# Kernel optimization log

Hardware: AMD Instinct MI355X
Metric: run time of the kernel (lower is better)

Reference implementation:

```python
import jax, jax.numpy as jnp
import numpy as np

WS = 3          # window size (odd)
NH = 8          # num heads
EPS = 1e-5      # LayerNorm eps (torch default)


def _ln(x, g, b):
    mu = x.mean(-1, keepdims=True)
    var = ((x - mu) ** 2).mean(-1, keepdims=True)
    return (x - mu) / jnp.sqrt(var + EPS) * g + b


def _neighbors(x, ws):
    # x: [B,D,H,W,C] -> [B,D,H,W,ws^3,C] zero-padded cubic neighborhoods
    B, D, H, W, C = x.shape
    r = ws // 2
    xp = jnp.pad(x, ((0, 0), (r, r), (r, r), (r, r), (0, 0)))
    slabs = [xp[:, i:i + D, j:j + H, k:k + W, :]
             for i in range(ws) for j in range(ws) for k in range(ws)]
    return jnp.stack(slabs, axis=4)


def _mask(D, H, W, ws):
    # True for valid (in-bounds, non-center) neighbors: [D,H,W,ws^3]
    r = ws // 2
    valid = jnp.pad(jnp.ones((D, H, W), dtype=bool), ((r, r), (r, r), (r, r)))
    slabs = [valid[i:i + D, j:j + H, k:k + W]
             for i in range(ws) for j in range(ws) for k in range(ws)]
    m = jnp.stack(slabs, axis=3)
    center = r * ws * ws + r * ws + r  # self voxel is masked out
    return m.at[..., center].set(False)


def setup_inputs() -> dict:
    key = jax.random.key(0)
    ks = jax.random.split(key, 18)
    B, D, H, W, C = 2, 16, 16, 16, 256
    F = 4 * C
    s = 0.02
    inp = {
        "x": jax.random.normal(ks[0], (B, D, H, W, C), jnp.float32),
        "Wq": jax.random.normal(ks[1], (C, C), jnp.float32) * s,
        "bq": jnp.zeros((C,), jnp.float32),
        "Wk": jax.random.normal(ks[2], (C, C), jnp.float32) * s,
        "bk": jnp.zeros((C,), jnp.float32),
        "Wv": jax.random.normal(ks[3], (C, C), jnp.float32) * s,
        "bv": jnp.zeros((C,), jnp.float32),
        "Wo": jax.random.normal(ks[4], (C, C), jnp.float32) * s,
        "bo": jnp.zeros((C,), jnp.float32),
        "g1": jnp.ones((C,), jnp.float32),
        "b1": jnp.zeros((C,), jnp.float32),
        "g2": jnp.ones((C,), jnp.float32),
        "b2": jnp.zeros((C,), jnp.float32),
        "W1": jax.random.normal(ks[5], (C, F), jnp.float32) * s,
        "bf1": jnp.zeros((F,), jnp.float32),
        "W2": jax.random.normal(ks[6], (F, C), jnp.float32) * s,
        "bf2": jnp.zeros((C,), jnp.float32),
    }
    return inp


def reference(x, Wq, bq, Wk, bk, Wv, bv, Wo, bo, g1, b1, g2, b2, W1, bf1, W2, bf2):
    B, D, H, W, C = x.shape
    ws, nh = WS, NH
    hd = C // nh
    K = ws ** 3

    nb = _neighbors(x, ws)                                   # [B,D,H,W,K,C]
    m = _mask(D, H, W, ws)                                   # [D,H,W,K]

    tn = _ln(x, g1, b1)                                      # norm1 on target only
    q = (tn @ Wq + bq).reshape(B, D, H, W, nh, hd)
    k = (nb @ Wk + bk).reshape(B, D, H, W, K, nh, hd)        # keys from RAW neighbors
    v = (nb @ Wv + bv).reshape(B, D, H, W, K, nh, hd)

    scale = hd ** -0.5
    scores = jnp.einsum('bpqrne,bpqrkne->bpqrnk', q, k) * scale  # [B,D,H,W,nh,K]
    mb = m[None, :, :, :, None, :]
    scores = jnp.where(mb, scores, -jnp.inf)
    attn = jax.nn.softmax(scores, axis=-1)
    attn = jnp.where(jnp.isnan(attn), jnp.zeros_like(attn), attn)

    ao = jnp.einsum('bpqrnk,bpqrkne->bpqrne', attn, v).reshape(B, D, H, W, C)
    ao = ao @ Wo + bo

    t = x + ao                                                # residual (dropout = eval identity)
    h = jax.nn.gelu(_ln(t, g2, b2) @ W1 + bf1, approximate=False) @ W2 + bf2
    return t + h
```

## Files before the change

### kernel.cpp

```cpp
#include <hip/hip_runtime.h>

typedef __bf16 bf16x8 __attribute__((ext_vector_type(8)));
typedef float f32x4 __attribute__((ext_vector_type(4)));

#define DEV static __device__ __forceinline__

DEV unsigned short f2b(float f){
    unsigned int u = __float_as_uint(f);
    u += 0x7fffu + ((u >> 16) & 1u);
    return (unsigned short)(u >> 16);
}
DEV float b2f(unsigned short h){ return __uint_as_float(((unsigned int)h) << 16); }
DEV float blo(unsigned int u){ return __uint_as_float(u << 16); }
DEV float bhi(unsigned int u){ return __uint_as_float(u & 0xffff0000u); }
DEV float gelu_f(float x){ return 0.5f * x * (1.0f + erff(x * 0.7071067811865476f)); }

DEV void gload16(const unsigned short* g, unsigned short* l){
    __builtin_amdgcn_global_load_lds(
        (const __attribute__((address_space(1))) void*)g,
        (__attribute__((address_space(3))) void*)l, 16, 0, 0);
}

static constexpr int NROW = 8192;
static constexpr int C    = 256;
static constexpr int F    = 1024;
static constexpr float ATT_SCALE = 0.17677669529663688f;

__global__ __launch_bounds__(256)
void prep_ln_kernel(const float* __restrict__ Wq, const float* __restrict__ Wk,
                    const float* __restrict__ Wv, const float* __restrict__ Wo,
                    const float* __restrict__ W1, const float* __restrict__ W2,
                    const float* __restrict__ bq, const float* __restrict__ bk,
                    const float* __restrict__ bv,
                    unsigned short* __restrict__ WQT, unsigned short* __restrict__ WKT,
                    unsigned short* __restrict__ WVT, unsigned short* __restrict__ WOT,
                    unsigned short* __restrict__ W1T, unsigned short* __restrict__ W2T,
                    float* __restrict__ bqkv,
                    const float* __restrict__ x, const float* __restrict__ g1,
                    const float* __restrict__ b1,
                    unsigned short* __restrict__ tn, unsigned short* __restrict__ xb)
{
    const int tid = threadIdx.x;
    if (blockIdx.x < 192) {
        __shared__ unsigned short T[64][66];
        const int t = blockIdx.x;
        const float* src; unsigned short* dst;
        int ldw, ldt, r0, c0; float sc = 1.0f;
        if (t < 64) {
            const int m = t >> 4, sub = t & 15;
            src = (m == 0) ? Wq : (m == 1) ? Wk : (m == 2) ? Wv : Wo;
            dst = (m == 0) ? WQT : (m == 1) ? WKT : (m == 2) ? WVT : WOT;
            if (m == 0) sc = ATT_SCALE;
            ldw = 256; ldt = 256;
            r0 = (sub >> 2) * 64; c0 = (sub & 3) * 64;
        } else if (t < 128) {
            const int sub = t - 64;
            src = W1; dst = W1T; ldw = 1024; ldt = 256;
            r0 = (sub >> 4) * 64; c0 = (sub & 15) * 64;
        } else {
            const int sub = t - 128;
            src = W2; dst = W2T; ldw = 256; ldt = 1024;
            r0 = (sub >> 2) * 64; c0 = (sub & 3) * 64;
        }
        #pragma unroll
        for (int i = 0; i < 16; ++i) {
            const int rl = i * 4 + (tid >> 6), cl = tid & 63;
            T[rl][cl] = f2b(src[(size_t)(r0 + rl) * ldw + c0 + cl] * sc);
        }
        __syncthreads();
        #pragma unroll
        for (int j = 0; j < 16; ++j) {
            const int cl = j * 4 + (tid >> 6), rl = tid & 63;
            dst[(size_t)(c0 + cl) * ldt + r0 + rl] = T[rl][cl];
        }
    } else if (blockIdx.x == 192) {
        #pragma unroll
        for (int i = 0; i < 3; ++i) {
            const int v = i * 256 + tid;
            bqkv[v] = (v < 256) ? bq[v] * ATT_SCALE
                    : (v < 512) ? bk[v - 256] : bv[v - 512];
        }
    } else {
        const int row  = (blockIdx.x - 193) * 4 + (tid >> 6);
        const int lane = tid & 63;
        float4 v = ((const float4*)(x + (size_t)row * C))[lane];
        float s = v.x + v.y + v.z + v.w;
        #pragma unroll
        for (int m = 32; m >= 1; m >>= 1) s += __shfl_xor(s, m);
        const float mean = s * (1.0f / 256.0f);
        const float d0 = v.x - mean, d1 = v.y - mean, d2 = v.z - mean, d3 = v.w - mean;
        float s2 = d0 * d0 + d1 * d1 + d2 * d2 + d3 * d3;
        #pragma unroll
        for (int m = 32; m >= 1; m >>= 1) s2 += __shfl_xor(s2, m);
        const float rstd = rsqrtf(s2 * (1.0f / 256.0f) + 1e-5f);
        float4 gg = ((const float4*)g1)[lane];
        float4 bb = ((const float4*)b1)[lane];
        ushort4 o = { f2b(d0 * rstd * gg.x + bb.x), f2b(d1 * rstd * gg.y + bb.y),
                      f2b(d2 * rstd * gg.z + bb.z), f2b(d3 * rstd * gg.w + bb.w) };
        ((ushort4*)(tn + (size_t)row * C))[lane] = o;
        ushort4 xo = { f2b(v.x), f2b(v.y), f2b(v.z), f2b(v.w) };
        ((ushort4*)(xb + (size_t)row * C))[lane] = xo;
    }
}

__global__ __launch_bounds__(256)
void ln_kernel(const float* __restrict__ X, const float* __restrict__ g,
               const float* __restrict__ bta, unsigned short* __restrict__ OUT)
{
    const int row  = blockIdx.x * 4 + (threadIdx.x >> 6);
    const int lane = threadIdx.x & 63;
    float4 v = ((const float4*)(X + (size_t)row * C))[lane];
    float s = v.x + v.y + v.z + v.w;
    #pragma unroll
    for (int m = 32; m >= 1; m >>= 1) s += __shfl_xor(s, m);
    const float mean = s * (1.0f / 256.0f);
    const float d0 = v.x - mean, d1 = v.y - mean, d2 = v.z - mean, d3 = v.w - mean;
    float s2 = d0 * d0 + d1 * d1 + d2 * d2 + d3 * d3;
    #pragma unroll
    for (int m = 32; m >= 1; m >>= 1) s2 += __shfl_xor(s2, m);
    const float rstd = rsqrtf(s2 * (1.0f / 256.0f) + 1e-5f);
    float4 gg = ((const float4*)g)[lane];
    float4 bb = ((const float4*)bta)[lane];
    ushort4 o = { f2b(d0 * rstd * gg.x + bb.x), f2b(d1 * rstd * gg.y + bb.y),
                  f2b(d2 * rstd * gg.z + bb.z), f2b(d3 * rstd * gg.w + bb.w) };
    ((ushort4*)(OUT + (size_t)row * C))[lane] = o;
}

template<int K, int MODE>
DEV void gemm_body(const unsigned short* __restrict__ A, int m0,
                   const unsigned short* __restrict__ BTt,
                   const float* __restrict__ biast,
                   const float* __restrict__ res, void* __restrict__ outp,
                   int ldo, int ocol0,
                   unsigned short (&As)[2][4096], unsigned short (&Bs)[2][4096])
{
    constexpr int BK = 64, NKT = K / BK;
    const int tid  = threadIdx.x;
    const int lane = tid & 63, wid = tid >> 6;
    const int srow = tid >> 3;
    const int schk = (tid & 7) ^ (srow & 7);

    const unsigned short* Ag = A   + (size_t)(m0 + srow) * K + schk * 8;
    const unsigned short* Bg = BTt + (size_t)srow        * K + schk * 8;

    const int wbase = __builtin_amdgcn_readfirstlane(wid) * 512;

    gload16(Ag,          &As[0][wbase]);
    gload16(Ag + 32 * K, &As[0][wbase + 2048]);
    gload16(Bg,          &Bs[0][wbase]);
    gload16(Bg + 32 * K, &Bs[0][wbase + 2048]);
    __syncthreads();

    f32x4 acc[4] = {};
    const int lr = lane & 15, lk = lane >> 4;
    const int sw = lr & 7;

    for (int kt = 0; kt < NKT; ++kt) {
        if (kt + 1 < NKT) {
            const int nb = (kt + 1) & 1;
            gload16(Ag + (kt + 1) * BK,          &As[nb][wbase]);
            gload16(Ag + 32 * K + (kt + 1) * BK, &As[nb][wbase + 2048]);
            gload16(Bg + (kt + 1) * BK,          &Bs[nb][wbase]);
            gload16(Bg + 32 * K + (kt + 1) * BK, &Bs[nb][wbase + 2048]);
        }
        const unsigned short* as = As[kt & 1];
        const unsigned short* bs = Bs[kt & 1];
        #pragma unroll
        for (int s = 0; s < 2; ++s) {
            const int c16 = (s * 4 + lk) ^ sw;
            bf16x8 bfr = *reinterpret_cast<const bf16x8*>(&bs[(wid * 16 + lr) * 64 + c16 * 8]);
            #pragma unroll
            for (int m = 0; m < 4; ++m) {
                bf16x8 afr = *reinterpret_cast<const bf16x8*>(&as[(m * 16 + lr) * 64 + c16 * 8]);
                acc[m] = __builtin_amdgcn_mfma_f32_16x16x32_bf16(afr, bfr, acc[m], 0, 0, 0);
            }
        }
        if (kt + 1 < NKT) __syncthreads();
    }

    const int col  = ocol0 + wid * 16 + lr;
    const float bcol = biast[wid * 16 + lr];
    #pragma unroll
    for (int m = 0; m < 4; ++m) {
        #pragma unroll
        for (int r = 0; r < 4; ++r) {
            const int row = m0 + m * 16 + lk * 4 + r;
            float v = acc[m][r] + bcol;
            if (MODE == 0) {
                ((unsigned short*)outp)[(size_t)row * ldo + col] = f2b(v);
            } else if (MODE == 1) {
                ((unsigned short*)outp)[(size_t)row * ldo + col] = f2b(gelu_f(v));
            } else {
                v += res[(size_t)row * ldo + col];
                ((float*)outp)[(size_t)row * ldo + col] = v;
            }
        }
    }
}

template<int NC, int TS>
DEV void tile_map(int& m0, int& n0){
    const int nwg = gridDim.x;
    const int lin = blockIdx.x;
    const int tile = (lin & 7) * (nwg >> 3) + (lin >> 3);
    m0 = (tile / NC) * TS;
    n0 = (tile % NC) * TS;
}

__global__ __launch_bounds__(256)
void qkv_kernel(const unsigned short* __restrict__ tn,
                const unsigned short* __restrict__ xb,
                const unsigned short* __restrict__ WT,
                const float* __restrict__ bqkv,
                unsigned short* __restrict__ QKV)
{
    __shared__ unsigned short As[2][4096], Bs[2][4096];
    int m0, n0; tile_map<12, 64>(m0, n0);
    const unsigned short* A = (n0 < 256) ? tn : xb;
    gemm_body<256, 0>(A, m0, WT + (size_t)n0 * 256,
                      bqkv + n0, nullptr, QKV, 768, n0, As, Bs);
}

template<int K, int MODE, int NC>
__global__ __launch_bounds__(256)
void gemm_kernel(const unsigned short* __restrict__ A,
                 const unsigned short* __restrict__ BT,
                 const float* __restrict__ bias,
                 const float* __restrict__ res,
                 void* __restrict__ outp, int ldo)
{
    __shared__ unsigned short As[2][4096], Bs[2][4096];
    int m0, n0; tile_map<NC, 64>(m0, n0);
    gemm_body<K, MODE>(A, m0, BT + (size_t)n0 * K,
                       bias + n0, res, outp, ldo, n0, As, Bs);
}

DEV float dot8(unsigned int x, unsigned int y, unsigned int z, unsigned int w,
               const float* q, float s){
    s = fmaf(q[0], blo(x), s); s = fmaf(q[1], bhi(x), s);
    s = fmaf(q[2], blo(y), s); s = fmaf(q[3], bhi(y), s);
    s = fmaf(q[4], blo(z), s); s = fmaf(q[5], bhi(z), s);
    s = fmaf(q[6], blo(w), s); s = fmaf(q[7], bhi(w), s);
    return s;
}
DEV void pv8(unsigned int x, unsigned int y, unsigned int z, unsigned int w,
             float p, float* a){
    a[0] = fmaf(p, blo(x), a[0]); a[1] = fmaf(p, bhi(x), a[1]);
    a[2] = fmaf(p, blo(y), a[2]); a[3] = fmaf(p, bhi(y), a[3]);
    a[4] = fmaf(p, blo(z), a[4]); a[5] = fmaf(p, bhi(z), a[5]);
    a[6] = fmaf(p, blo(w), a[6]); a[7] = fmaf(p, bhi(w), a[7]);
}

__global__ __launch_bounds__(256, 1)
void attn_kernel(const unsigned short* __restrict__ QKV,
                 unsigned short* __restrict__ AO)
{
    const int t    = blockIdx.x * 256 + threadIdx.x;
    const int vox  = t >> 3;
    const int head = t & 7;
    const int d = (vox >> 8) & 15, h = (vox >> 4) & 15, w = vox & 15;
    const int ch = head * 32;

    float q[32];
    {
        const uint4* qp = reinterpret_cast<const uint4*>(&QKV[(size_t)vox * 768 + ch]);
        uint4 u0 = qp[0], u1 = qp[1], u2 = qp[2], u3 = qp[3];
        q[0]=blo(u0.x); q[1]=bhi(u0.x); q[2]=blo(u0.y); q[3]=bhi(u0.y);
        q[4]=blo(u0.z); q[5]=bhi(u0.z); q[6]=blo(u0.w); q[7]=bhi(u0.w);
        q[8]=blo(u1.x); q[9]=bhi(u1.x); q[10]=blo(u1.y); q[11]=bhi(u1.y);
        q[12]=blo(u1.z); q[13]=bhi(u1.z); q[14]=blo(u1.w); q[15]=bhi(u1.w);
        q[16]=blo(u2.x); q[17]=bhi(u2.x); q[18]=blo(u2.y); q[19]=bhi(u2.y);
        q[20]=blo(u2.z); q[21]=bhi(u2.z); q[22]=blo(u2.w); q[23]=bhi(u2.w);
        q[24]=blo(u3.x); q[25]=bhi(u3.x); q[26]=blo(u3.y); q[27]=bhi(u3.y);
        q[28]=blo(u3.z); q[29]=bhi(u3.z); q[30]=blo(u3.w); q[31]=bhi(u3.w);
    }

    float sc[27];
    int   nr[27];
    #pragma unroll
    for (int kk = 0; kk < 27; ++kk) {
        const int di = kk / 9 - 1, hi2 = (kk / 3) % 3 - 1, wi = kk % 3 - 1;
        const int nd = d + di, nh = h + hi2, nw = w + wi;
        const bool valid = (kk != 13) && ((unsigned)nd < 16u) &&
                           ((unsigned)nh < 16u) && ((unsigned)nw < 16u);
        const int r = valid ? ((vox & 4096) | (nd << 8) | (nh << 4) | nw) : vox;
        nr[kk] = r;
        const uint4* kp = reinterpret_cast<const uint4*>(&QKV[(size_t)r * 768 + 256 + ch]);
        uint4 u0 = kp[0], u1 = kp[1], u2 = kp[2], u3 = kp[3];
        float s = 0.0f;
        s = dot8(u0.x, u0.y, u0.z, u0.w, q + 0,  s);
        s = dot8(u1.x, u1.y, u1.z, u1.w, q + 8,  s);
        s = dot8(u2.x, u2.y, u2.z, u2.w, q + 16, s);
        s = dot8(u3.x, u3.y, u3.z, u3.w, q + 24, s);
        sc[kk] = valid ? s : -INFINITY;
    }

    float mx = sc[0];
    #pragma unroll
    for (int kk = 1; kk < 27; ++kk) mx = fmaxf(mx, sc[kk]);
    float z = 0.0f;
    #pragma unroll
    for (int kk = 0; kk < 27; ++kk) { float p = __expf(sc[kk] - mx); sc[kk] = p; z += p; }
    const float inv = 1.0f / z;

    float acc[32] = {};
    #pragma unroll
    for (int kk = 0; kk < 27; ++kk) {
        const uint4* vp = reinterpret_cast<const uint4*>(&QKV[(size_t)nr[kk] * 768 + 512 + ch]);
        uint4 u0 = vp[0], u1 = vp[1], u2 = vp[2], u3 = vp[3];
        const float p = sc[kk];
        pv8(u0.x, u0.y, u0.z, u0.w, p, acc + 0);
        pv8(u1.x, u1.y, u1.z, u1.w, p, acc + 8);
        pv8(u2.x, u2.y, u2.z, u2.w, p, acc + 16);
        pv8(u3.x, u3.y, u3.z, u3.w, p, acc + 24);
    }

    uint4* op = reinterpret_cast<uint4*>(&AO[(size_t)vox * C + ch]);
    #pragma unroll
    for (int i = 0; i < 4; ++i) {
        uint4 o;
        o.x = (unsigned)f2b(acc[i*8+0] * inv) | ((unsigned)f2b(acc[i*8+1] * inv) << 16);
        o.y = (unsigned)f2b(acc[i*8+2] * inv) | ((unsigned)f2b(acc[i*8+3] * inv) << 16);
        o.z = (unsigned)f2b(acc[i*8+4] * inv) | ((unsigned)f2b(acc[i*8+5] * inv) << 16);
        o.w = (unsigned)f2b(acc[i*8+6] * inv) | ((unsigned)f2b(acc[i*8+7] * inv) << 16);
        op[i] = o;
    }
}

extern "C" void kernel_launch(void* const* d_in, const int* in_sizes, int n_in,
                              void* d_out, int out_size, void* d_ws, size_t ws_size,
                              hipStream_t stream)
{
    const float* x   = (const float*)d_in[0];
    const float* Wq  = (const float*)d_in[1];
    const float* bq  = (const float*)d_in[2];
    const float* Wk  = (const float*)d_in[3];
    const float* bk  = (const float*)d_in[4];
    const float* Wv  = (const float*)d_in[5];
    const float* bv  = (const float*)d_in[6];
    const float* Wo  = (const float*)d_in[7];
    const float* bo  = (const float*)d_in[8];
    const float* g1  = (const float*)d_in[9];
    const float* b1  = (const float*)d_in[10];
    const float* g2  = (const float*)d_in[11];
    const float* b2  = (const float*)d_in[12];
    const float* W1  = (const float*)d_in[13];
    const float* bf1 = (const float*)d_in[14];
    const float* W2  = (const float*)d_in[15];
    const float* bf2 = (const float*)d_in[16];

    char* ws = (char*)d_ws;
    size_t o = 0;
    unsigned short* WQT = (unsigned short*)(ws + o); o += (size_t)256 * 256 * 2;
    unsigned short* WKT = (unsigned short*)(ws + o); o += (size_t)256 * 256 * 2;
    unsigned short* WVT = (unsigned short*)(ws + o); o += (size_t)256 * 256 * 2;
    unsigned short* WOT = (unsigned short*)(ws + o); o += (size_t)256 * 256 * 2;
    unsigned short* W1T = (unsigned short*)(ws + o); o += (size_t)256 * 1024 * 2;
    unsigned short* W2T = (unsigned short*)(ws + o); o += (size_t)1024 * 256 * 2;
    float*          bqkv= (float*)(ws + o);          o += (size_t)768 * 4;
    unsigned short* tn  = (unsigned short*)(ws + o); o += (size_t)NROW * C * 2;
    unsigned short* xb  = (unsigned short*)(ws + o); o += (size_t)NROW * C * 2;
    unsigned short* QKVb= (unsigned short*)(ws + o); o += (size_t)NROW * 768 * 2;
    unsigned short* AOb = (unsigned short*)(ws + o); o += (size_t)NROW * C * 2;
    float*          Tf  = (float*)(ws + o);          o += (size_t)NROW * C * 4;
    unsigned short* tn2 = (unsigned short*)(ws + o); o += (size_t)NROW * C * 2;
    unsigned short* Hb  = (unsigned short*)(ws + o); o += (size_t)NROW * F * 2;

    prep_ln_kernel<<<193 + NROW / 4, 256, 0, stream>>>(Wq, Wk, Wv, Wo, W1, W2, bq, bk, bv,
                                                       WQT, WKT, WVT, WOT, W1T, W2T, bqkv,
                                                       x, g1, b1, tn, xb);

    qkv_kernel<<<(NROW / 64) * 12, 256, 0, stream>>>(tn, xb, WQT, bqkv, QKVb);

    attn_kernel<<<NROW * 8 / 256, 256, 0, stream>>>(QKVb, AOb);

    gemm_kernel<256, 2, 4><<<(NROW / 64) * 4, 256, 0, stream>>>(AOb, WOT, bo, x, Tf, 256);

    ln_kernel<<<NROW / 4, 256, 0, stream>>>(Tf, g2, b2, tn2);

    gemm_kernel<256, 1, 16><<<(NROW / 64) * 16, 256, 0, stream>>>(tn2, W1T, bf1, nullptr, Hb, 1024);

    gemm_kernel<1024, 2, 4><<<(NROW / 64) * 4, 256, 0, stream>>>(Hb, W2T, bf2, Tf, (float*)d_out, 256);
}
```

Measured before the change: 76.89 us.

## Split attention head across 4 threads with shuffle-reduced dot products

The attention kernel now assigns 8 channels per thread, so 4 threads share one head, instead of one thread handling a whole 32-channel head. Partial q·k dot products are combined with xor shuffles. The change cuts registers per thread, raises the occupancy hint to 4 blocks, and launches 4x as many threads, with neighboring lanes issuing coalesced 16-byte loads. The cost is two shuffles per neighbor, and the softmax work is now repeated in each of the 4 lanes.

```diff
diff --git a/kernel.cpp b/kernel.cpp
--- a/kernel.cpp
+++ b/kernel.cpp
@@ -235,44 +235,29 @@
                        bias + n0, res, outp, ldo, n0, As, Bs);
 }
 
-DEV float dot8(unsigned int x, unsigned int y, unsigned int z, unsigned int w,
-               const float* q, float s){
-    s = fmaf(q[0], blo(x), s); s = fmaf(q[1], bhi(x), s);
-    s = fmaf(q[2], blo(y), s); s = fmaf(q[3], bhi(y), s);
-    s = fmaf(q[4], blo(z), s); s = fmaf(q[5], bhi(z), s);
-    s = fmaf(q[6], blo(w), s); s = fmaf(q[7], bhi(w), s);
+DEV float dot8(uint4 u, const float* q){
+    float s;
+    s = q[0] * blo(u.x);          s = fmaf(q[1], bhi(u.x), s);
+    s = fmaf(q[2], blo(u.y), s);  s = fmaf(q[3], bhi(u.y), s);
+    s = fmaf(q[4], blo(u.z), s);  s = fmaf(q[5], bhi(u.z), s);
+    s = fmaf(q[6], blo(u.w), s);  s = fmaf(q[7], bhi(u.w), s);
     return s;
 }
-DEV void pv8(unsigned int x, unsigned int y, unsigned int z, unsigned int w,
-             float p, float* a){
-    a[0] = fmaf(p, blo(x), a[0]); a[1] = fmaf(p, bhi(x), a[1]);
-    a[2] = fmaf(p, blo(y), a[2]); a[3] = fmaf(p, bhi(y), a[3]);
-    a[4] = fmaf(p, blo(z), a[4]); a[5] = fmaf(p, bhi(z), a[5]);
-    a[6] = fmaf(p, blo(w), a[6]); a[7] = fmaf(p, bhi(w), a[7]);
-}
-
-__global__ __launch_bounds__(256, 1)
+
+__global__ __launch_bounds__(256, 4)
 void attn_kernel(const unsigned short* __restrict__ QKV,
                  unsigned short* __restrict__ AO)
 {
-    const int t    = blockIdx.x * 256 + threadIdx.x;
-    const int vox  = t >> 3;
-    const int head = t & 7;
+    const int t   = blockIdx.x * 256 + threadIdx.x;
+    const int vox = t >> 5;
+    const int ch  = (t & 31) * 8;
     const int d = (vox >> 8) & 15, h = (vox >> 4) & 15, w = vox & 15;
-    const int ch = head * 32;
-
-    float q[32];
+
+    float q[8];
     {
-        const uint4* qp = reinterpret_cast<const uint4*>(&QKV[(size_t)vox * 768 + ch]);
-        uint4 u0 = qp[0], u1 = qp[1], u2 = qp[2], u3 = qp[3];
-        q[0]=blo(u0.x); q[1]=bhi(u0.x); q[2]=blo(u0.y); q[3]=bhi(u0.y);
-        q[4]=blo(u0.z); q[5]=bhi(u0.z); q[6]=blo(u0.w); q[7]=bhi(u0.w);
-        q[8]=blo(u1.x); q[9]=bhi(u1.x); q[10]=blo(u1.y); q[11]=bhi(u1.y);
-        q[12]=blo(u1.z); q[13]=bhi(u1.z); q[14]=blo(u1.w); q[15]=bhi(u1.w);
-        q[16]=blo(u2.x); q[17]=bhi(u2.x); q[18]=blo(u2.y); q[19]=bhi(u2.y);
-        q[20]=blo(u2.z); q[21]=bhi(u2.z); q[22]=blo(u2.w); q[23]=bhi(u2.w);
-        q[24]=blo(u3.x); q[25]=bhi(u3.x); q[26]=blo(u3.y); q[27]=bhi(u3.y);
-        q[28]=blo(u3.z); q[29]=bhi(u3.z); q[30]=blo(u3.w); q[31]=bhi(u3.w);
+        uint4 u = *reinterpret_cast<const uint4*>(&QKV[(size_t)vox * 768 + ch]);
+        q[0]=blo(u.x); q[1]=bhi(u.x); q[2]=blo(u.y); q[3]=bhi(u.y);
+        q[4]=blo(u.z); q[5]=bhi(u.z); q[6]=blo(u.w); q[7]=bhi(u.w);
     }
 
     float sc[27];
@@ -285,13 +270,10 @@
                            ((unsigned)nh < 16u) && ((unsigned)nw < 16u);
         const int r = valid ? ((vox & 4096) | (nd << 8) | (nh << 4) | nw) : vox;
         nr[kk] = r;
-        const uint4* kp = reinterpret_cast<const uint4*>(&QKV[(size_t)r * 768 + 256 + ch]);
-        uint4 u0 = kp[0], u1 = kp[1], u2 = kp[2], u3 = kp[3];
-        float s = 0.0f;
-        s = dot8(u0.x, u0.y, u0.z, u0.w, q + 0,  s);
-        s = dot8(u1.x, u1.y, u1.z, u1.w, q + 8,  s);
-        s = dot8(u2.x, u2.y, u2.z, u2.w, q + 16, s);
-        s = dot8(u3.x, u3.y, u3.z, u3.w, q + 24, s);
+        uint4 u = *reinterpret_cast<const uint4*>(&QKV[(size_t)r * 768 + 256 + ch]);
+        float s = dot8(u, q);
+        s += __shfl_xor(s, 1);
+        s += __shfl_xor(s, 2);
         sc[kk] = valid ? s : -INFINITY;
     }
 
@@ -303,28 +285,23 @@
     for (int kk = 0; kk < 27; ++kk) { float p = __expf(sc[kk] - mx); sc[kk] = p; z += p; }
     const float inv = 1.0f / z;
 
-    float acc[32] = {};
+    float acc[8] = {};
     #pragma unroll
     for (int kk = 0; kk < 27; ++kk) {
-        const uint4* vp = reinterpret_cast<const uint4*>(&QKV[(size_t)nr[kk] * 768 + 512 + ch]);
-        uint4 u0 = vp[0], u1 = vp[1], u2 = vp[2], u3 = vp[3];
+        uint4 u = *reinterpret_cast<const uint4*>(&QKV[(size_t)nr[kk] * 768 + 512 + ch]);
         const float p = sc[kk];
-        pv8(u0.x, u0.y, u0.z, u0.w, p, acc + 0);
-        pv8(u1.x, u1.y, u1.z, u1.w, p, acc + 8);
-        pv8(u2.x, u2.y, u2.z, u2.w, p, acc + 16);
-        pv8(u3.x, u3.y, u3.z, u3.w, p, acc + 24);
-    }
-
-    uint4* op = reinterpret_cast<uint4*>(&AO[(size_t)vox * C + ch]);
-    #pragma unroll
-    for (int i = 0; i < 4; ++i) {
-        uint4 o;
-        o.x = (unsigned)f2b(acc[i*8+0] * inv) | ((unsigned)f2b(acc[i*8+1] * inv) << 16);
-        o.y = (unsigned)f2b(acc[i*8+2] * inv) | ((unsigned)f2b(acc[i*8+3] * inv) << 16);
-        o.z = (unsigned)f2b(acc[i*8+4] * inv) | ((unsigned)f2b(acc[i*8+5] * inv) << 16);
-        o.w = (unsigned)f2b(acc[i*8+6] * inv) | ((unsigned)f2b(acc[i*8+7] * inv) << 16);
-        op[i] = o;
-    }
+        acc[0] = fmaf(p, blo(u.x), acc[0]); acc[1] = fmaf(p, bhi(u.x), acc[1]);
+        acc[2] = fmaf(p, blo(u.y), acc[2]); acc[3] = fmaf(p, bhi(u.y), acc[3]);
+        acc[4] = fmaf(p, blo(u.z), acc[4]); acc[5] = fmaf(p, bhi(u.z), acc[5]);
+        acc[6] = fmaf(p, blo(u.w), acc[6]); acc[7] = fmaf(p, bhi(u.w), acc[7]);
+    }
+
+    uint4 o;
+    o.x = (unsigned)f2b(acc[0] * inv) | ((unsigned)f2b(acc[1] * inv) << 16);
+    o.y = (unsigned)f2b(acc[2] * inv) | ((unsigned)f2b(acc[3] * inv) << 16);
+    o.z = (unsigned)f2b(acc[4] * inv) | ((unsigned)f2b(acc[5] * inv) << 16);
+    o.w = (unsigned)f2b(acc[6] * inv) | ((unsigned)f2b(acc[7] * inv) << 16);
+    *reinterpret_cast<uint4*>(&AO[(size_t)vox * C + ch]) = o;
 }
 
 extern "C" void kernel_launch(void* const* d_in, const int* in_sizes, int n_in,
@@ -372,7 +349,7 @@
 
     qkv_kernel<<<(NROW / 64) * 12, 256, 0, stream>>>(tn, xb, WQT, bqkv, QKVb);
 
-    attn_kernel<<<NROW * 8 / 256, 256, 0, stream>>>(QKVb, AOb);
+    attn_kernel<<<NROW * 32 / 256, 256, 0, stream>>>(QKVb, AOb);
 
     gemm_kernel<256, 2, 4><<<(NROW / 64) * 4, 256, 0, stream>>>(AOb, WOT, bo, x, Tf, 256);
 
```

Result: slower. 81.18 us (+5.6%).
